# Kernel optimization log

Measured on AMD Instinct MI355X. Metric: run time of the kernel, lower is better.

The kernel has to match this reference:

```python
import jax, jax.numpy as jnp
import numpy as np

C, B, N, IN, OUT = 32, 32, 4096, 16, 32
NUM_ITERS = 3


def _squash(t, axis=-1):
    # scale = |t|^2 / (1 + |t|^2); out = scale * t / |t|
    sn = jnp.sum(t * t, axis=axis, keepdims=True)
    return (sn / (1.0 + sn)) * t / jnp.sqrt(sn)


def setup_inputs() -> dict:
    key = jax.random.key(0)
    k1, k2 = jax.random.split(key)
    x = jax.random.normal(k1, (B, N, IN), dtype=jnp.float32)
    route_weights = jax.random.normal(k2, (C, N, IN, OUT), dtype=jnp.float32)
    return {"x": x, "route_weights": route_weights}


def reference(x, route_weights):
    # priors[c,b,n,d] = sum_i x[b,n,i] * W[c,n,i,d]  (torch: [C,B,N,1,D], singleton dropped)
    priors = jnp.einsum('bni,cnio->cbno', x, route_weights)  # [C,B,N,D]
    # torch logits are [C,B,N,1,D] but constant over D (delta broadcasts), and the
    # custom softmax normalizes over dim=2 (route nodes N), so [C,B,N] is equivalent.
    logits = jnp.zeros(priors.shape[:3], dtype=priors.dtype)  # [C,B,N]
    outputs = None
    for i in range(NUM_ITERS):
        probs = jax.nn.softmax(logits, axis=2)  # softmax over route nodes (dim=2)
        s = jnp.sum(probs[..., None] * priors, axis=2, keepdims=True)  # [C,B,1,D]
        outputs = _squash(s, axis=-1)
        if i != NUM_ITERS - 1:
            logits = logits + jnp.sum(priors * outputs, axis=-1)  # agreement [C,B,N]
    return outputs[:, :, :, None, :]  # [C,B,1,1,D] to match torch output shape
```

## Files before the change

### kernel.cpp

```cpp
#include <hip/hip_runtime.h>
#include <hip/hip_cooperative_groups.h>
#include <math.h>

namespace cg = cooperative_groups;


typedef _Float16 f16x8 __attribute__((ext_vector_type(8)));
typedef float f32x16 __attribute__((ext_vector_type(16)));

namespace {
constexpr int kC = 32, kB = 32, kN = 4096, kI = 16, kD = 32;
constexpr int CHUNKS = 32;
constexpr int CHUNK_N = kN / CHUNKS;
constexpr int PS = kB * kD + kB;
constexpr int GRID = kC * CHUNKS;
constexpr size_t XT_ELEMS = (size_t)kN * kB * kI;
constexpr size_t WT_ELEMS = (size_t)kC * kN * kI * kD;
constexpr size_t P_FLOATS = (size_t)kC * CHUNKS * PS;
constexpr size_t CV_FLOATS = (size_t)kC * kB * kD;
constexpr size_t WS_BYTES_MID = XT_ELEMS * 2 + (P_FLOATS + CV_FLOATS) * 4;
constexpr size_t WS_BYTES_BIG =
    (XT_ELEMS + WT_ELEMS) * 2 + (P_FLOATS + CV_FLOATS) * 4;
constexpr size_t WS_BYTES_COOP =
    (XT_ELEMS + WT_ELEMS) * 2 + (3 * P_FLOATS + 2 * CV_FLOATS) * 4;
}

__device__ __forceinline__ f32x16 zero16() {
  f32x16 z;
#pragma unroll
  for (int r = 0; r < 16; ++r) z[r] = 0.f;
  return z;
}

__global__ __launch_bounds__(256) void k_xt(const float* __restrict__ x,
                                            _Float16* __restrict__ xt) {
  const int t = blockIdx.x * 256 + threadIdx.x;
  const int r = t >> 1, half = t & 1;
  const int b = r >> 12, n = r & 4095;
  const float4* s4 =
      reinterpret_cast<const float4*>(x) + (size_t)r * 4 + half * 2;
  const float4 f0 = s4[0], f1 = s4[1];
  f16x8 o;
  o[0] = (_Float16)f0.x; o[1] = (_Float16)f0.y;
  o[2] = (_Float16)f0.z; o[3] = (_Float16)f0.w;
  o[4] = (_Float16)f1.x; o[5] = (_Float16)f1.y;
  o[6] = (_Float16)f1.z; o[7] = (_Float16)f1.w;
  *reinterpret_cast<f16x8*>(xt + ((size_t)n * kB + b) * kI + half * 8) = o;
}


__device__ __forceinline__ void mega_sweep0(const float* __restrict__ W,
                                            const _Float16* __restrict__ xt,
                                            _Float16* __restrict__ Wt,
                                            float* __restrict__ P,
                                            float (*red)[32][33], int c,
                                            int chunk, int tid) {
  const int w = tid >> 6, l = tid & 63;
  const int m = l & 31, h = l >> 5;
  const int n0 = chunk * CHUNK_N;
  constexpr int TILES = CHUNK_N / 4;

  const float* wp = W + ((size_t)c * kN + n0 + w) * 512 + (h * 8) * 32 + m;
  const _Float16* xp = xt + ((size_t)(n0 + w)) * 512 + m * 16 + h * 8;
  _Float16* wtp = Wt + ((size_t)c * kN + n0 + w) * 512 + (size_t)l * 8;

  f32x16 accA = zero16(), accB = zero16();

  float rA0[8], rA1[8];
  f16x8 B0, B1;
#pragma unroll
  for (int j = 0; j < 8; ++j) rA0[j] = __builtin_nontemporal_load(wp + j * 32);
  B0 = *reinterpret_cast<const f16x8*>(xp);
#pragma unroll
  for (int j = 0; j < 8; ++j)
    rA1[j] = __builtin_nontemporal_load(wp + 2048 + j * 32);
  B1 = *reinterpret_cast<const f16x8*>(xp + 2048);

#pragma unroll 1
  for (int t = 0; t < TILES; t += 2) {
    {
      f16x8 a;
#pragma unroll
      for (int j = 0; j < 8; ++j) a[j] = (_Float16)rA0[j];
      const f16x8 b = B0;
      const int tn = (t + 2 < TILES) ? t + 2 : 0;
#pragma unroll
      for (int j = 0; j < 8; ++j)
        rA0[j] = __builtin_nontemporal_load(wp + (size_t)tn * 2048 + j * 32);
      B0 = *reinterpret_cast<const f16x8*>(xp + (size_t)tn * 2048);
      *reinterpret_cast<f16x8*>(wtp + (size_t)t * 2048) = a;
      accA = __builtin_amdgcn_mfma_f32_32x32x16_f16(a, b, accA, 0, 0, 0);
    }
    {
      f16x8 a;
#pragma unroll
      for (int j = 0; j < 8; ++j) a[j] = (_Float16)rA1[j];
      const f16x8 b = B1;
      const int tn = (t + 3 < TILES) ? t + 3 : 0;
#pragma unroll
      for (int j = 0; j < 8; ++j)
        rA1[j] = __builtin_nontemporal_load(wp + (size_t)tn * 2048 + j * 32);
      B1 = *reinterpret_cast<const f16x8*>(xp + (size_t)tn * 2048);
      *reinterpret_cast<f16x8*>(wtp + (size_t)(t + 1) * 2048) = a;
      accB = __builtin_amdgcn_mfma_f32_32x32x16_f16(a, b, accB, 0, 0, 0);
    }
  }
#pragma unroll
  for (int r = 0; r < 16; ++r) accA[r] += accB[r];

#pragma unroll
  for (int r = 0; r < 16; ++r)
    red[w][(r & 3) + 8 * (r >> 2) + 4 * h][m] = accA[r];
  __syncthreads();

  float* Pp = P + ((size_t)c * CHUNKS + chunk) * PS;
#pragma unroll
  for (int e = tid; e < 1024; e += 256) {
    const int d = e >> 5, bb = e & 31;
    Pp[e] = red[0][d][bb] + red[1][d][bb] + red[2][d][bb] + red[3][d][bb];
  }
  __syncthreads();
}

__device__ __forceinline__ void mega_sweep_wt(
    const _Float16* __restrict__ Wt, const _Float16* __restrict__ xt,
    const float* __restrict__ cumVec, float* __restrict__ P,
    float (*red)[32][33], float (*lred)[32], int c, int chunk, int tid) {
  const int w = tid >> 6, l = tid & 63;
  const int m = l & 31, h = l >> 5;
  const int n0 = chunk * CHUNK_N;
  constexpr int TILES = CHUNK_N / 4;

  const _Float16* wp = Wt + ((size_t)c * kN + n0 + w) * 512 + (size_t)l * 8;
  const _Float16* xp = xt + ((size_t)(n0 + w)) * 512 + m * 16 + h * 8;

  float cvr[16];
  const float* cvp = cumVec + (size_t)c * 1024 + m * 32;
#pragma unroll
  for (int r = 0; r < 16; ++r) cvr[r] = cvp[(r & 3) + 8 * (r >> 2) + 4 * h];

  f32x16 accA = zero16(), accB = zero16();
  float lacc = 0.f;
  const f32x16 z = zero16();

  f16x8 A0, A1, B0, B1;
  A0 = *reinterpret_cast<const f16x8*>(wp);
  B0 = *reinterpret_cast<const f16x8*>(xp);
  A1 = *reinterpret_cast<const f16x8*>(wp + 2048);
  B1 = *reinterpret_cast<const f16x8*>(xp + 2048);

#pragma unroll 1
  for (int t = 0; t < TILES; t += 2) {
    {
      const f16x8 a = A0;
      const f16x8 b = B0;
      const int tn = (t + 2 < TILES) ? t + 2 : 0;
      A0 = *reinterpret_cast<const f16x8*>(wp + (size_t)tn * 2048);
      B0 = *reinterpret_cast<const f16x8*>(xp + (size_t)tn * 2048);
      const f32x16 pr =
          __builtin_amdgcn_mfma_f32_32x32x16_f16(a, b, z, 0, 0, 0);
      float d0 = pr[0] * cvr[0], d1 = pr[1] * cvr[1];
      float d2 = pr[2] * cvr[2], d3 = pr[3] * cvr[3];
#pragma unroll
      for (int r = 4; r < 16; r += 4) {
        d0 = fmaf(pr[r + 0], cvr[r + 0], d0);
        d1 = fmaf(pr[r + 1], cvr[r + 1], d1);
        d2 = fmaf(pr[r + 2], cvr[r + 2], d2);
        d3 = fmaf(pr[r + 3], cvr[r + 3], d3);
      }
      float dp = (d0 + d1) + (d2 + d3);
      dp += __shfl_xor(dp, 32);
      const float e = __expf(dp);
      lacc += e;
#pragma unroll
      for (int r = 0; r < 16; ++r) accA[r] = fmaf(e, pr[r], accA[r]);
    }
    {
      const f16x8 a = A1;
      const f16x8 b = B1;
      const int tn = (t + 3 < TILES) ? t + 3 : 0;
      A1 = *reinterpret_cast<const f16x8*>(wp + (size_t)tn * 2048);
      B1 = *reinterpret_cast<const f16x8*>(xp + (size_t)tn * 2048);
      const f32x16 pr =
          __builtin_amdgcn_mfma_f32_32x32x16_f16(a, b, z, 0, 0, 0);
      float d0 = pr[0] * cvr[0], d1 = pr[1] * cvr[1];
      float d2 = pr[2] * cvr[2], d3 = pr[3] * cvr[3];
#pragma unroll
      for (int r = 4; r < 16; r += 4) {
        d0 = fmaf(pr[r + 0], cvr[r + 0], d0);
        d1 = fmaf(pr[r + 1], cvr[r + 1], d1);
        d2 = fmaf(pr[r + 2], cvr[r + 2], d2);
        d3 = fmaf(pr[r + 3], cvr[r + 3], d3);
      }
      float dp = (d0 + d1) + (d2 + d3);
      dp += __shfl_xor(dp, 32);
      const float e = __expf(dp);
      lacc += e;
#pragma unroll
      for (int r = 0; r < 16; ++r) accB[r] = fmaf(e, pr[r], accB[r]);
    }
  }
#pragma unroll
  for (int r = 0; r < 16; ++r) accA[r] += accB[r];

#pragma unroll
  for (int r = 0; r < 16; ++r)
    red[w][(r & 3) + 8 * (r >> 2) + 4 * h][m] = accA[r];
  if (h == 0) lred[w][m] = lacc;
  __syncthreads();

  float* Pp = P + ((size_t)c * CHUNKS + chunk) * PS;
#pragma unroll
  for (int e = tid; e < 1024; e += 256) {
    const int d = e >> 5, bb = e & 31;
    Pp[e] = red[0][d][bb] + red[1][d][bb] + red[2][d][bb] + red[3][d][bb];
  }
  if (tid < 32)
    Pp[1024 + tid] = lred[0][tid] + lred[1][tid] + lred[2][tid] + lred[3][tid];
  __syncthreads();
}

template <int K>
__device__ __forceinline__ void mega_reduce(const float* __restrict__ P,
                                            float* __restrict__ CVout,
                                            float* __restrict__ out,
                                            float (&cvrun)[4], int c, int t) {
  const int b = t >> 3, dg = t & 7;
  const float* Pc = P + (size_t)c * CHUNKS * PS;
  float s0 = 0.f, s1 = 0.f, s2 = 0.f, s3 = 0.f, lb = 0.f;
#pragma unroll 4
  for (int ch = 0; ch < CHUNKS; ++ch) {
    const float* base = Pc + (size_t)ch * PS;
    s0 += base[(dg + 0) * 32 + b];
    s1 += base[(dg + 8) * 32 + b];
    s2 += base[(dg + 16) * 32 + b];
    s3 += base[(dg + 24) * 32 + b];
    if (K != 0 && dg == 0) lb += base[1024 + b];
  }
  float inv;
  if constexpr (K == 0) {
    inv = 1.0f / (float)kN;
  } else {
    lb = __shfl(lb, (t & 63) & 56);
    inv = 1.0f / lb;
  }
  const float v0 = s0 * inv, v1 = s1 * inv, v2 = s2 * inv, v3 = s3 * inv;
  float sn = v0 * v0 + v1 * v1 + v2 * v2 + v3 * v3;
  sn += __shfl_xor(sn, 1);
  sn += __shfl_xor(sn, 2);
  sn += __shfl_xor(sn, 4);
  const float coef = sqrtf(sn) / (1.0f + sn);
  const size_t o0 = (size_t)c * 1024 + b * 32 + dg;
  if constexpr (K == 0) {
    cvrun[0] = v0 * coef; cvrun[1] = v1 * coef;
    cvrun[2] = v2 * coef; cvrun[3] = v3 * coef;
    CVout[o0 + 0] = cvrun[0];  CVout[o0 + 8] = cvrun[1];
    CVout[o0 + 16] = cvrun[2]; CVout[o0 + 24] = cvrun[3];
  } else if constexpr (K == 1) {
    cvrun[0] += v0 * coef; cvrun[1] += v1 * coef;
    cvrun[2] += v2 * coef; cvrun[3] += v3 * coef;
    CVout[o0 + 0] = cvrun[0];  CVout[o0 + 8] = cvrun[1];
    CVout[o0 + 16] = cvrun[2]; CVout[o0 + 24] = cvrun[3];
  } else {
    out[o0 + 0] = v0 * coef;  out[o0 + 8] = v1 * coef;
    out[o0 + 16] = v2 * coef; out[o0 + 24] = v3 * coef;
  }
}

__global__ __launch_bounds__(256, 4) void k_mega(
    const float* __restrict__ W, const _Float16* __restrict__ xt,
    _Float16* __restrict__ Wt, float* __restrict__ P0, float* __restrict__ P1,
    float* __restrict__ P2, float* __restrict__ CVa, float* __restrict__ CVb,
    float* __restrict__ out) {
  __shared__ float red[4][32][33];
  __shared__ float lred[4][32];
  cg::grid_group grid = cg::this_grid();
  const int bid = blockIdx.x;
  const int c = bid & 31;
  const int chunk = bid >> 5;
  const int tid = threadIdx.x;
  float cvrun[4] = {0.f, 0.f, 0.f, 0.f};

  mega_sweep0(W, xt, Wt, P0, red, c, chunk, tid);
  __threadfence();
  grid.sync();

  if (bid < 32) mega_reduce<0>(P0, CVa, nullptr, cvrun, bid, tid);
  __threadfence();
  grid.sync();

  mega_sweep_wt(Wt, xt, CVa, P1, red, lred, c, chunk, tid);
  __threadfence();
  grid.sync();

  if (bid < 32) mega_reduce<1>(P1, CVb, nullptr, cvrun, bid, tid);
  __threadfence();
  grid.sync();

  mega_sweep_wt(Wt, xt, CVb, P2, red, lred, c, chunk, tid);
  __threadfence();
  grid.sync();

  if (bid < 32) mega_reduce<2>(P2, nullptr, out, cvrun, bid, tid);
}


template <int MODE, bool EMIT>
__global__ __launch_bounds__(256) void k_sweep(const float* __restrict__ W,
                                               const _Float16* __restrict__ xt,
                                               const float* __restrict__ cumVec,
                                               float* __restrict__ partials,
                                               _Float16* __restrict__ Wt) {
  __shared__ float red[4][32][33];
  __shared__ float lred[4][32];
  const int bid = blockIdx.x;
  const int c = bid & 31;
  const int chunk = bid >> 5;
  const int tid = threadIdx.x;
  const int w = tid >> 6, l = tid & 63;
  const int m = l & 31, h = l >> 5;
  const int n0 = chunk * CHUNK_N;
  constexpr int TILES = CHUNK_N / 4;

  const float* wp = W + ((size_t)c * kN + n0 + w) * 512 + (h * 8) * 32 + m;
  const _Float16* xp = xt + ((size_t)(n0 + w)) * 512 + m * 16 + h * 8;
  _Float16* wtp =
      EMIT ? (Wt + ((size_t)c * kN + n0 + w) * 512 + (size_t)l * 8) : nullptr;

  float cvr[16];
  if (MODE) {
    const float* cvp = cumVec + (size_t)c * 1024 + m * 32;
#pragma unroll
    for (int r = 0; r < 16; ++r) cvr[r] = cvp[(r & 3) + 8 * (r >> 2) + 4 * h];
  }

  f32x16 accA = zero16(), accB = zero16();
  float lacc = 0.f;
  const f32x16 z = zero16();

  float rA0[8], rA1[8];
  f16x8 B0, B1;
#pragma unroll
  for (int j = 0; j < 8; ++j)
    rA0[j] = EMIT ? __builtin_nontemporal_load(wp + j * 32) : wp[j * 32];
  B0 = *reinterpret_cast<const f16x8*>(xp);
#pragma unroll
  for (int j = 0; j < 8; ++j)
    rA1[j] = EMIT ? __builtin_nontemporal_load(wp + 2048 + j * 32)
                  : wp[2048 + j * 32];
  B1 = *reinterpret_cast<const f16x8*>(xp + 2048);

#pragma unroll 1
  for (int t = 0; t < TILES; t += 2) {
    {
      f16x8 a;
#pragma unroll
      for (int j = 0; j < 8; ++j) a[j] = (_Float16)rA0[j];
      const f16x8 b = B0;
      const int tn = (t + 2 < TILES) ? t + 2 : 0;
#pragma unroll
      for (int j = 0; j < 8; ++j)
        rA0[j] = EMIT ? __builtin_nontemporal_load(wp + (size_t)tn * 2048 +
                                                   j * 32)
                      : wp[(size_t)tn * 2048 + j * 32];
      B0 = *reinterpret_cast<const f16x8*>(xp + (size_t)tn * 2048);
      if constexpr (EMIT)
        *reinterpret_cast<f16x8*>(wtp + (size_t)t * 2048) = a;
      if constexpr (MODE == 0) {
        accA = __builtin_amdgcn_mfma_f32_32x32x16_f16(a, b, accA, 0, 0, 0);
      } else {
        const f32x16 pr =
            __builtin_amdgcn_mfma_f32_32x32x16_f16(a, b, z, 0, 0, 0);
        float d0 = pr[0] * cvr[0], d1 = pr[1] * cvr[1];
        float d2 = pr[2] * cvr[2], d3 = pr[3] * cvr[3];
#pragma unroll
        for (int r = 4; r < 16; r += 4) {
          d0 = fmaf(pr[r + 0], cvr[r + 0], d0);
          d1 = fmaf(pr[r + 1], cvr[r + 1], d1);
          d2 = fmaf(pr[r + 2], cvr[r + 2], d2);
          d3 = fmaf(pr[r + 3], cvr[r + 3], d3);
        }
        float dp = (d0 + d1) + (d2 + d3);
        dp += __shfl_xor(dp, 32);
        const float e = __expf(dp);
        lacc += e;
#pragma unroll
        for (int r = 0; r < 16; ++r) accA[r] = fmaf(e, pr[r], accA[r]);
      }
    }
    {
      f16x8 a;
#pragma unroll
      for (int j = 0; j < 8; ++j) a[j] = (_Float16)rA1[j];
      const f16x8 b = B1;
      const int tn = (t + 3 < TILES) ? t + 3 : 0;
#pragma unroll
      for (int j = 0; j < 8; ++j)
        rA1[j] = EMIT ? __builtin_nontemporal_load(wp + (size_t)tn * 2048 +
                                                   j * 32)
                      : wp[(size_t)tn * 2048 + j * 32];
      B1 = *reinterpret_cast<const f16x8*>(xp + (size_t)tn * 2048);
      if constexpr (EMIT)
        *reinterpret_cast<f16x8*>(wtp + (size_t)(t + 1) * 2048) = a;
      if constexpr (MODE == 0) {
        accB = __builtin_amdgcn_mfma_f32_32x32x16_f16(a, b, accB, 0, 0, 0);
      } else {
        const f32x16 pr =
            __builtin_amdgcn_mfma_f32_32x32x16_f16(a, b, z, 0, 0, 0);
        float d0 = pr[0] * cvr[0], d1 = pr[1] * cvr[1];
        float d2 = pr[2] * cvr[2], d3 = pr[3] * cvr[3];
#pragma unroll
        for (int r = 4; r < 16; r += 4) {
          d0 = fmaf(pr[r + 0], cvr[r + 0], d0);
          d1 = fmaf(pr[r + 1], cvr[r + 1], d1);
          d2 = fmaf(pr[r + 2], cvr[r + 2], d2);
          d3 = fmaf(pr[r + 3], cvr[r + 3], d3);
        }
        float dp = (d0 + d1) + (d2 + d3);
        dp += __shfl_xor(dp, 32);
        const float e = __expf(dp);
        lacc += e;
#pragma unroll
        for (int r = 0; r < 16; ++r) accB[r] = fmaf(e, pr[r], accB[r]);
      }
    }
  }
#pragma unroll
  for (int r = 0; r < 16; ++r) accA[r] += accB[r];

#pragma unroll
  for (int r = 0; r < 16; ++r)
    red[w][(r & 3) + 8 * (r >> 2) + 4 * h][m] = accA[r];
  if (MODE && h == 0) lred[w][m] = lacc;
  __syncthreads();

  float* Pp = partials + ((size_t)c * CHUNKS + chunk) * PS;
#pragma unroll
  for (int e = tid; e < 1024; e += 256) {
    const int d = e >> 5, bb = e & 31;
    Pp[e] = red[0][d][bb] + red[1][d][bb] + red[2][d][bb] + red[3][d][bb];
  }
  if (MODE && tid < 32)
    Pp[1024 + tid] = lred[0][tid] + lred[1][tid] + lred[2][tid] + lred[3][tid];
}

__global__ __launch_bounds__(256) void k_sweep_wt(
    const _Float16* __restrict__ Wt, const _Float16* __restrict__ xt,
    const float* __restrict__ cumVec, float* __restrict__ partials) {
  __shared__ float red[4][32][33];
  __shared__ float lred[4][32];
  const int bid = blockIdx.x;
  const int c = bid & 31;
  const int chunk = bid >> 5;
  const int tid = threadIdx.x;
  mega_sweep_wt(Wt, xt, cumVec, partials, red, lred, c, chunk, tid);
}

template <int K>
__global__ __launch_bounds__(1024) void k_reduce(
    const float* __restrict__ partials, float* __restrict__ CV,
    float* __restrict__ out) {
  const int c = blockIdx.x;
  const int t = threadIdx.x;
  const int b = t >> 5, d = t & 31;
  const float* Pc = partials + (size_t)c * CHUNKS * PS;
  float s = 0.f;
#pragma unroll 4
  for (int ch = 0; ch < CHUNKS; ++ch) s += Pc[(size_t)ch * PS + d * 32 + b];
  float inv;
  if constexpr (K == 0) {
    inv = 1.0f / (float)kN;
  } else {
    float lb = 0.f;
#pragma unroll 4
    for (int ch = 0; ch < CHUNKS; ++ch) lb += Pc[(size_t)ch * PS + 1024 + b];
    inv = 1.0f / lb;
  }
  const float sv = s * inv;
  float sn = sv * sv;
  sn += __shfl_xor(sn, 1);
  sn += __shfl_xor(sn, 2);
  sn += __shfl_xor(sn, 4);
  sn += __shfl_xor(sn, 8);
  sn += __shfl_xor(sn, 16);
  const float coef = sqrtf(sn) / (1.0f + sn);
  const float o = sv * coef;
  if constexpr (K == 2)
    out[(size_t)c * 1024 + t] = o;
  else if constexpr (K == 0)
    CV[(size_t)c * 1024 + t] = o;
  else
    CV[(size_t)c * 1024 + t] += o;
}

namespace v1 {
constexpr int BG = 4, NSLOT = 128, THREADS1 = NSLOT * 8;
template <int MODE>
__device__ __forceinline__ void sweep_pass(const float* __restrict__ Wc,
                                           const float* __restrict__ x, int b0,
                                           int tid, int nslot, int dg,
                                           float (*red)[8][20], float (*sS)[kD],
                                           float* sL, const float (*sVec)[kD]) {
  float acc[BG][4];
  float lv[BG];
#pragma unroll
  for (int b = 0; b < BG; ++b) {
    lv[b] = 0.f;
#pragma unroll
    for (int j = 0; j < 4; ++j) acc[b][j] = 0.f;
  }
  float vec[BG][4];
  if (MODE) {
#pragma unroll
    for (int b = 0; b < BG; ++b)
#pragma unroll
      for (int j = 0; j < 4; ++j) vec[b][j] = sVec[b][4 * dg + j];
  }
#pragma unroll 1
  for (int n = nslot; n < kN; n += NSLOT) {
    const float* Wn = Wc + (size_t)n * (kI * kD) + 4 * dg;
    float pr[BG][4];
#pragma unroll
    for (int b = 0; b < BG; ++b)
#pragma unroll
      for (int j = 0; j < 4; ++j) pr[b][j] = 0.f;
#pragma unroll
    for (int iq = 0; iq < 4; ++iq) {
      float4 wv[4];
#pragma unroll
      for (int r = 0; r < 4; ++r)
        wv[r] = *reinterpret_cast<const float4*>(Wn + (4 * iq + r) * kD);
#pragma unroll
      for (int b = 0; b < BG; ++b) {
        const float4 xv = *reinterpret_cast<const float4*>(
            x + ((size_t)(b0 + b) * kN + n) * kI + 4 * iq);
        const float xsv[4] = {xv.x, xv.y, xv.z, xv.w};
#pragma unroll
        for (int r = 0; r < 4; ++r) {
          pr[b][0] = fmaf(xsv[r], wv[r].x, pr[b][0]);
          pr[b][1] = fmaf(xsv[r], wv[r].y, pr[b][1]);
          pr[b][2] = fmaf(xsv[r], wv[r].z, pr[b][2]);
          pr[b][3] = fmaf(xsv[r], wv[r].w, pr[b][3]);
        }
      }
    }
    if (MODE == 0) {
#pragma unroll
      for (int b = 0; b < BG; ++b)
#pragma unroll
        for (int j = 0; j < 4; ++j) acc[b][j] += pr[b][j];
    } else {
#pragma unroll
      for (int b = 0; b < BG; ++b) {
        float dp = pr[b][0] * vec[b][0] + pr[b][1] * vec[b][1] +
                   pr[b][2] * vec[b][2] + pr[b][3] * vec[b][3];
        dp += __shfl_xor(dp, 1);
        dp += __shfl_xor(dp, 2);
        dp += __shfl_xor(dp, 4);
        const float e = __expf(dp);
        lv[b] += e;
        acc[b][0] = fmaf(e, pr[b][0], acc[b][0]);
        acc[b][1] = fmaf(e, pr[b][1], acc[b][1]);
        acc[b][2] = fmaf(e, pr[b][2], acc[b][2]);
        acc[b][3] = fmaf(e, pr[b][3], acc[b][3]);
      }
    }
  }
#pragma unroll
  for (int b = 0; b < BG; ++b) {
#pragma unroll
    for (int j = 0; j < 4; ++j) {
      float v = acc[b][j];
      v += __shfl_xor(v, 8);
      v += __shfl_xor(v, 16);
      v += __shfl_xor(v, 32);
      acc[b][j] = v;
    }
    if (MODE) {
      float v = lv[b];
      v += __shfl_xor(v, 8);
      v += __shfl_xor(v, 16);
      v += __shfl_xor(v, 32);
      lv[b] = v;
    }
  }
  const int lane = tid & 63;
  const int wv_id = tid >> 6;
  if ((lane >> 3) == 0) {
#pragma unroll
    for (int b = 0; b < BG; ++b) {
#pragma unroll
      for (int j = 0; j < 4; ++j) red[wv_id][dg][4 * b + j] = acc[b][j];
      if (MODE) red[wv_id][dg][16 + b] = lv[b];
    }
  }
  __syncthreads();
  if (tid < 128) {
    const int dgc = tid >> 4, e = tid & 15;
    float s = 0.f;
#pragma unroll
    for (int w = 0; w < 16; ++w) s += red[w][dgc][e];
    sS[e >> 2][4 * dgc + (e & 3)] = s;
  }
  if (MODE && tid >= 128 && tid < 128 + BG) {
    const int b = tid - 128;
    float s = 0.f;
#pragma unroll
    for (int w = 0; w < 16; ++w) s += red[w][0][16 + b];
    sL[b] = s;
  }
  __syncthreads();
}

__global__ __launch_bounds__(THREADS1, 4) void caps_route_kernel(
    const float* __restrict__ x, const float* __restrict__ W,
    float* __restrict__ out) {
  __shared__ float red[16][8][20];
  __shared__ float sS[BG][kD];
  __shared__ float sVec[BG][kD];
  __shared__ float sL[BG];
  const int i = blockIdx.x;
  const int xcd = i & 7;
  const int j = i >> 3;
  const int c = xcd + 8 * (j >> 3);
  const int b0 = 4 * (j & 7);
  const int tid = threadIdx.x;
  const int nslot = tid >> 3;
  const int dg = tid & 7;
  const float* Wc = W + (size_t)c * kN * kI * kD;
  sweep_pass<0>(Wc, x, b0, tid, nslot, dg, red, sS, sL, sVec);
  if (tid < BG) {
    const int b = tid;
    float sval[kD], sn = 0.f;
    const float inv = 1.0f / (float)kN;
#pragma unroll
    for (int d = 0; d < kD; ++d) {
      sval[d] = sS[b][d] * inv;
      sn += sval[d] * sval[d];
    }
    const float coef = sqrtf(sn) / (1.0f + sn);
#pragma unroll
    for (int d = 0; d < kD; ++d) sVec[b][d] = sval[d] * coef;
  }
  __syncthreads();
  sweep_pass<1>(Wc, x, b0, tid, nslot, dg, red, sS, sL, sVec);
  if (tid < BG) {
    const int b = tid;
    float sval[kD], sn = 0.f;
    const float inv = 1.0f / sL[b];
#pragma unroll
    for (int d = 0; d < kD; ++d) {
      sval[d] = sS[b][d] * inv;
      sn += sval[d] * sval[d];
    }
    const float coef = sqrtf(sn) / (1.0f + sn);
#pragma unroll
    for (int d = 0; d < kD; ++d) sVec[b][d] += sval[d] * coef;
  }
  __syncthreads();
  sweep_pass<1>(Wc, x, b0, tid, nslot, dg, red, sS, sL, sVec);
  if (tid < BG) {
    const int b = tid;
    float sval[kD], sn = 0.f;
    const float inv = 1.0f / sL[b];
#pragma unroll
    for (int d = 0; d < kD; ++d) {
      sval[d] = sS[b][d] * inv;
      sn += sval[d] * sval[d];
    }
    const float coef = sqrtf(sn) / (1.0f + sn);
    float* o = out + ((size_t)c * kB + (b0 + b)) * kD;
#pragma unroll
    for (int d = 0; d < kD; ++d) o[d] = sval[d] * coef;
  }
}
}

extern "C" void kernel_launch(void* const* d_in, const int* in_sizes, int n_in,
                              void* d_out, int out_size, void* d_ws,
                              size_t ws_size, hipStream_t stream) {
  const float* x = (const float*)d_in[0];
  const float* W = (const float*)d_in[1];
  float* out = (float*)d_out;
  (void)in_sizes; (void)n_in; (void)out_size;

  static int s_coop = -1;
  if (s_coop < 0) {
    int dev = 0;
    (void)hipGetDevice(&dev);
    int nCU = 0;
    (void)hipDeviceGetAttribute(&nCU, hipDeviceAttributeMultiprocessorCount,
                                dev);
    int maxB = 0;
    (void)hipOccupancyMaxActiveBlocksPerMultiprocessor(&maxB, k_mega, 256, 0);
    s_coop = (nCU > 0 && maxB > 0 && (size_t)nCU * maxB >= (size_t)GRID) ? 1
                                                                         : 0;
  }

  if (s_coop == 1 && ws_size >= WS_BYTES_COOP) {
    _Float16* xt = (_Float16*)d_ws;
    _Float16* Wt = xt + XT_ELEMS;
    float* P0 = (float*)(Wt + WT_ELEMS);
    float* P1 = P0 + P_FLOATS;
    float* P2 = P1 + P_FLOATS;
    float* CVa = P2 + P_FLOATS;
    float* CVb = CVa + CV_FLOATS;

    k_xt<<<GRID, 256, 0, stream>>>(x, xt);
    void* args[] = {(void*)&W,  (void*)&xt,  (void*)&Wt,
                    (void*)&P0, (void*)&P1,  (void*)&P2,
                    (void*)&CVa, (void*)&CVb, (void*)&out};
    if (hipLaunchCooperativeKernel(k_mega, dim3(GRID), dim3(256), args, 0,
                                   stream) == hipSuccess)
      return;
  }

  if (ws_size >= WS_BYTES_BIG) {
    _Float16* xt = (_Float16*)d_ws;
    _Float16* Wt = xt + XT_ELEMS;
    float* P = (float*)(Wt + WT_ELEMS);
    float* CV = P + P_FLOATS;

    k_xt<<<GRID, 256, 0, stream>>>(x, xt);
    k_sweep<0, true><<<GRID, 256, 0, stream>>>(W, xt, nullptr, P, Wt);
    k_reduce<0><<<kC, 1024, 0, stream>>>(P, CV, nullptr);
    k_sweep_wt<<<GRID, 256, 0, stream>>>(Wt, xt, CV, P);
    k_reduce<1><<<kC, 1024, 0, stream>>>(P, CV, nullptr);
    k_sweep_wt<<<GRID, 256, 0, stream>>>(Wt, xt, CV, P);
    k_reduce<2><<<kC, 1024, 0, stream>>>(P, nullptr, out);
    return;
  }

  if (ws_size >= WS_BYTES_MID) {
    _Float16* xt = (_Float16*)d_ws;
    float* P = (float*)(xt + XT_ELEMS);
    float* CV = P + P_FLOATS;

    k_xt<<<GRID, 256, 0, stream>>>(x, xt);
    k_sweep<0, false><<<GRID, 256, 0, stream>>>(W, xt, nullptr, P, nullptr);
    k_reduce<0><<<kC, 1024, 0, stream>>>(P, CV, nullptr);
    k_sweep<1, false><<<GRID, 256, 0, stream>>>(W, xt, CV, P, nullptr);
    k_reduce<1><<<kC, 1024, 0, stream>>>(P, CV, nullptr);
    k_sweep<1, false><<<GRID, 256, 0, stream>>>(W, xt, CV, P, nullptr);
    k_reduce<2><<<kC, 1024, 0, stream>>>(P, nullptr, out);
    return;
  }

  v1::caps_route_kernel<<<256, v1::THREADS1, 0, stream>>>(x, W, out);
}
```

Measured before the change: 200.9 us.

## Replace cooperative grid syncs with per-capsule atomic barriers and redundant reductions

The cooperative-launch grid.sync barriers are replaced by a hand-built two-level atomic counter barrier, reset by the xt conversion kernel. Every block now redundantly reduces its own capsule's partials into shared memory, so the separate reduce phase and its extra grid barrier go away. Only the final output reduction waits again, and only in chunk-0 blocks. This removes barrier overhead and the serialized reduce stage, at the cost of redundant reduction reads and reliance on all blocks being co-resident under a normal launch.

```diff
diff --git a/kernel.cpp b/kernel.cpp
--- a/kernel.cpp
+++ b/kernel.cpp
@@ -1,8 +1,5 @@
 #include <hip/hip_runtime.h>
-#include <hip/hip_cooperative_groups.h>
 #include <math.h>
-
-namespace cg = cooperative_groups;
 
 
 typedef _Float16 f16x8 __attribute__((ext_vector_type(8)));
@@ -18,11 +15,12 @@
 constexpr size_t WT_ELEMS = (size_t)kC * kN * kI * kD;
 constexpr size_t P_FLOATS = (size_t)kC * CHUNKS * PS;
 constexpr size_t CV_FLOATS = (size_t)kC * kB * kD;
+constexpr int BAR_U32 = 33;
 constexpr size_t WS_BYTES_MID = XT_ELEMS * 2 + (P_FLOATS + CV_FLOATS) * 4;
 constexpr size_t WS_BYTES_BIG =
     (XT_ELEMS + WT_ELEMS) * 2 + (P_FLOATS + CV_FLOATS) * 4;
-constexpr size_t WS_BYTES_COOP =
-    (XT_ELEMS + WT_ELEMS) * 2 + (3 * P_FLOATS + 2 * CV_FLOATS) * 4;
+constexpr size_t WS_BYTES_MEGA =
+    (XT_ELEMS + WT_ELEMS) * 2 + 3 * P_FLOATS * 4 + 256;
 }
 
 __device__ __forceinline__ f32x16 zero16() {
@@ -33,7 +31,9 @@
 }
 
 __global__ __launch_bounds__(256) void k_xt(const float* __restrict__ x,
-                                            _Float16* __restrict__ xt) {
+                                            _Float16* __restrict__ xt,
+                                            unsigned* __restrict__ bar) {
+  if (bar && blockIdx.x == 0 && threadIdx.x < BAR_U32) bar[threadIdx.x] = 0u;
   const int t = blockIdx.x * 256 + threadIdx.x;
   const int r = t >> 1, half = t & 1;
   const int b = r >> 12, n = r & 4095;
@@ -48,6 +48,29 @@
   *reinterpret_cast<f16x8*>(xt + ((size_t)n * kB + b) * kI + half * 8) = o;
 }
 
+__device__ __forceinline__ void bar_arrive(unsigned* bar, int bid, int tid) {
+  __threadfence();
+  __syncthreads();
+  if (tid == 0) {
+    const int g = bid & 31;
+    unsigned v = __hip_atomic_fetch_add(&bar[g], 1u, __ATOMIC_ACQ_REL,
+                                        __HIP_MEMORY_SCOPE_AGENT);
+    if ((v & 31u) == 31u)
+      __hip_atomic_fetch_add(&bar[32], 1u, __ATOMIC_ACQ_REL,
+                             __HIP_MEMORY_SCOPE_AGENT);
+  }
+}
+
+__device__ __forceinline__ void bar_wait(unsigned* bar, int tid, int epoch) {
+  if (tid == 0) {
+    const unsigned target = 32u * (unsigned)epoch;
+    while (__hip_atomic_load(&bar[32], __ATOMIC_ACQUIRE,
+                             __HIP_MEMORY_SCOPE_AGENT) < target)
+      __builtin_amdgcn_s_sleep(2);
+  }
+  __syncthreads();
+}
+
 
 __device__ __forceinline__ void mega_sweep0(const float* __restrict__ W,
                                             const _Float16* __restrict__ xt,
@@ -119,13 +142,12 @@
     const int d = e >> 5, bb = e & 31;
     Pp[e] = red[0][d][bb] + red[1][d][bb] + red[2][d][bb] + red[3][d][bb];
   }
-  __syncthreads();
 }
 
 __device__ __forceinline__ void mega_sweep_wt(
     const _Float16* __restrict__ Wt, const _Float16* __restrict__ xt,
-    const float* __restrict__ cumVec, float* __restrict__ P,
-    float (*red)[32][33], float (*lred)[32], int c, int chunk, int tid) {
+    const float (*sCV)[32], float* __restrict__ P, float (*red)[32][33],
+    float (*lred)[32], int c, int chunk, int tid) {
   const int w = tid >> 6, l = tid & 63;
   const int m = l & 31, h = l >> 5;
   const int n0 = chunk * CHUNK_N;
@@ -135,9 +157,9 @@
   const _Float16* xp = xt + ((size_t)(n0 + w)) * 512 + m * 16 + h * 8;
 
   float cvr[16];
-  const float* cvp = cumVec + (size_t)c * 1024 + m * 32;
-#pragma unroll
-  for (int r = 0; r < 16; ++r) cvr[r] = cvp[(r & 3) + 8 * (r >> 2) + 4 * h];
+#pragma unroll
+  for (int r = 0; r < 16; ++r)
+    cvr[r] = sCV[m][(r & 3) + 8 * (r >> 2) + 4 * h];
 
   f32x16 accA = zero16(), accB = zero16();
   float lacc = 0.f;
@@ -217,25 +239,30 @@
   }
   if (tid < 32)
     Pp[1024 + tid] = lred[0][tid] + lred[1][tid] + lred[2][tid] + lred[3][tid];
-  __syncthreads();
 }
 
 template <int K>
 __device__ __forceinline__ void mega_reduce(const float* __restrict__ P,
-                                            float* __restrict__ CVout,
                                             float* __restrict__ out,
-                                            float (&cvrun)[4], int c, int t) {
+                                            float (&cvrun)[4],
+                                            float (*sCV)[32], int c, int t) {
   const int b = t >> 3, dg = t & 7;
   const float* Pc = P + (size_t)c * CHUNKS * PS;
   float s0 = 0.f, s1 = 0.f, s2 = 0.f, s3 = 0.f, lb = 0.f;
 #pragma unroll 4
   for (int ch = 0; ch < CHUNKS; ++ch) {
     const float* base = Pc + (size_t)ch * PS;
-    s0 += base[(dg + 0) * 32 + b];
-    s1 += base[(dg + 8) * 32 + b];
-    s2 += base[(dg + 16) * 32 + b];
-    s3 += base[(dg + 24) * 32 + b];
-    if (K != 0 && dg == 0) lb += base[1024 + b];
+    s0 += __hip_atomic_load(base + (dg + 0) * 32 + b, __ATOMIC_RELAXED,
+                            __HIP_MEMORY_SCOPE_AGENT);
+    s1 += __hip_atomic_load(base + (dg + 8) * 32 + b, __ATOMIC_RELAXED,
+                            __HIP_MEMORY_SCOPE_AGENT);
+    s2 += __hip_atomic_load(base + (dg + 16) * 32 + b, __ATOMIC_RELAXED,
+                            __HIP_MEMORY_SCOPE_AGENT);
+    s3 += __hip_atomic_load(base + (dg + 24) * 32 + b, __ATOMIC_RELAXED,
+                            __HIP_MEMORY_SCOPE_AGENT);
+    if (K != 0 && dg == 0)
+      lb += __hip_atomic_load(base + 1024 + b, __ATOMIC_RELAXED,
+                              __HIP_MEMORY_SCOPE_AGENT);
   }
   float inv;
   if constexpr (K == 0) {
@@ -250,31 +277,31 @@
   sn += __shfl_xor(sn, 2);
   sn += __shfl_xor(sn, 4);
   const float coef = sqrtf(sn) / (1.0f + sn);
-  const size_t o0 = (size_t)c * 1024 + b * 32 + dg;
-  if constexpr (K == 0) {
-    cvrun[0] = v0 * coef; cvrun[1] = v1 * coef;
-    cvrun[2] = v2 * coef; cvrun[3] = v3 * coef;
-    CVout[o0 + 0] = cvrun[0];  CVout[o0 + 8] = cvrun[1];
-    CVout[o0 + 16] = cvrun[2]; CVout[o0 + 24] = cvrun[3];
-  } else if constexpr (K == 1) {
-    cvrun[0] += v0 * coef; cvrun[1] += v1 * coef;
-    cvrun[2] += v2 * coef; cvrun[3] += v3 * coef;
-    CVout[o0 + 0] = cvrun[0];  CVout[o0 + 8] = cvrun[1];
-    CVout[o0 + 16] = cvrun[2]; CVout[o0 + 24] = cvrun[3];
-  } else {
+  if constexpr (K == 2) {
+    const size_t o0 = (size_t)c * 1024 + b * 32 + dg;
     out[o0 + 0] = v0 * coef;  out[o0 + 8] = v1 * coef;
     out[o0 + 16] = v2 * coef; out[o0 + 24] = v3 * coef;
-  }
-}
-
-__global__ __launch_bounds__(256, 4) void k_mega(
+  } else {
+    if constexpr (K == 0) {
+      cvrun[0] = v0 * coef; cvrun[1] = v1 * coef;
+      cvrun[2] = v2 * coef; cvrun[3] = v3 * coef;
+    } else {
+      cvrun[0] += v0 * coef; cvrun[1] += v1 * coef;
+      cvrun[2] += v2 * coef; cvrun[3] += v3 * coef;
+    }
+    sCV[b][dg + 0] = cvrun[0];  sCV[b][dg + 8] = cvrun[1];
+    sCV[b][dg + 16] = cvrun[2]; sCV[b][dg + 24] = cvrun[3];
+  }
+}
+
+__global__ __launch_bounds__(256, 4) void k_mega2(
     const float* __restrict__ W, const _Float16* __restrict__ xt,
     _Float16* __restrict__ Wt, float* __restrict__ P0, float* __restrict__ P1,
-    float* __restrict__ P2, float* __restrict__ CVa, float* __restrict__ CVb,
+    float* __restrict__ P2, unsigned* __restrict__ bar,
     float* __restrict__ out) {
   __shared__ float red[4][32][33];
   __shared__ float lred[4][32];
-  cg::grid_group grid = cg::this_grid();
+  __shared__ float sCV[32][32];
   const int bid = blockIdx.x;
   const int c = bid & 31;
   const int chunk = bid >> 5;
@@ -282,26 +309,26 @@
   float cvrun[4] = {0.f, 0.f, 0.f, 0.f};
 
   mega_sweep0(W, xt, Wt, P0, red, c, chunk, tid);
-  __threadfence();
-  grid.sync();
-
-  if (bid < 32) mega_reduce<0>(P0, CVa, nullptr, cvrun, bid, tid);
-  __threadfence();
-  grid.sync();
-
-  mega_sweep_wt(Wt, xt, CVa, P1, red, lred, c, chunk, tid);
-  __threadfence();
-  grid.sync();
-
-  if (bid < 32) mega_reduce<1>(P1, CVb, nullptr, cvrun, bid, tid);
-  __threadfence();
-  grid.sync();
-
-  mega_sweep_wt(Wt, xt, CVb, P2, red, lred, c, chunk, tid);
-  __threadfence();
-  grid.sync();
-
-  if (bid < 32) mega_reduce<2>(P2, nullptr, out, cvrun, bid, tid);
+  bar_arrive(bar, bid, tid);
+  bar_wait(bar, tid, 1);
+
+  mega_reduce<0>(P0, nullptr, cvrun, sCV, c, tid);
+  __syncthreads();
+
+  mega_sweep_wt(Wt, xt, sCV, P1, red, lred, c, chunk, tid);
+  bar_arrive(bar, bid, tid);
+  bar_wait(bar, tid, 2);
+
+  mega_reduce<1>(P1, nullptr, cvrun, sCV, c, tid);
+  __syncthreads();
+
+  mega_sweep_wt(Wt, xt, sCV, P2, red, lred, c, chunk, tid);
+  bar_arrive(bar, bid, tid);
+
+  if (chunk == 0) {
+    bar_wait(bar, tid, 3);
+    mega_reduce<2>(P2, out, cvrun, sCV, c, tid);
+  }
 }
 
 
@@ -449,11 +476,15 @@
     const float* __restrict__ cumVec, float* __restrict__ partials) {
   __shared__ float red[4][32][33];
   __shared__ float lred[4][32];
+  __shared__ float sCV[32][32];
   const int bid = blockIdx.x;
   const int c = bid & 31;
   const int chunk = bid >> 5;
   const int tid = threadIdx.x;
-  mega_sweep_wt(Wt, xt, cumVec, partials, red, lred, c, chunk, tid);
+  for (int e = tid; e < 1024; e += 256)
+    sCV[e >> 5][e & 31] = cumVec[(size_t)c * 1024 + e];
+  __syncthreads();
+  mega_sweep_wt(Wt, xt, sCV, partials, red, lred, c, chunk, tid);
 }
 
 template <int K>
@@ -684,35 +715,31 @@
   float* out = (float*)d_out;
   (void)in_sizes; (void)n_in; (void)out_size;
 
-  static int s_coop = -1;
-  if (s_coop < 0) {
+  static int s_mega = -1;
+  if (s_mega < 0) {
     int dev = 0;
     (void)hipGetDevice(&dev);
     int nCU = 0;
     (void)hipDeviceGetAttribute(&nCU, hipDeviceAttributeMultiprocessorCount,
                                 dev);
     int maxB = 0;
-    (void)hipOccupancyMaxActiveBlocksPerMultiprocessor(&maxB, k_mega, 256, 0);
-    s_coop = (nCU > 0 && maxB > 0 && (size_t)nCU * maxB >= (size_t)GRID) ? 1
-                                                                         : 0;
-  }
-
-  if (s_coop == 1 && ws_size >= WS_BYTES_COOP) {
+    (void)hipOccupancyMaxActiveBlocksPerMultiprocessor(&maxB, k_mega2, 256, 0);
+    s_mega = (nCU > 0 && maxB > 0 && (size_t)nCU * (size_t)maxB >= (size_t)GRID)
+                 ? 1
+                 : 0;
+  }
+
+  if (s_mega == 1 && ws_size >= WS_BYTES_MEGA) {
     _Float16* xt = (_Float16*)d_ws;
     _Float16* Wt = xt + XT_ELEMS;
     float* P0 = (float*)(Wt + WT_ELEMS);
     float* P1 = P0 + P_FLOATS;
     float* P2 = P1 + P_FLOATS;
-    float* CVa = P2 + P_FLOATS;
-    float* CVb = CVa + CV_FLOATS;
-
-    k_xt<<<GRID, 256, 0, stream>>>(x, xt);
-    void* args[] = {(void*)&W,  (void*)&xt,  (void*)&Wt,
-                    (void*)&P0, (void*)&P1,  (void*)&P2,
-                    (void*)&CVa, (void*)&CVb, (void*)&out};
-    if (hipLaunchCooperativeKernel(k_mega, dim3(GRID), dim3(256), args, 0,
-                                   stream) == hipSuccess)
-      return;
+    unsigned* bar = (unsigned*)(P2 + P_FLOATS);
+
+    k_xt<<<GRID, 256, 0, stream>>>(x, xt, bar);
+    k_mega2<<<GRID, 256, 0, stream>>>(W, xt, Wt, P0, P1, P2, bar, out);
+    return;
   }
 
   if (ws_size >= WS_BYTES_BIG) {
@@ -721,7 +748,7 @@
     float* P = (float*)(Wt + WT_ELEMS);
     float* CV = P + P_FLOATS;
 
-    k_xt<<<GRID, 256, 0, stream>>>(x, xt);
+    k_xt<<<GRID, 256, 0, stream>>>(x, xt, nullptr);
     k_sweep<0, true><<<GRID, 256, 0, stream>>>(W, xt, nullptr, P, Wt);
     k_reduce<0><<<kC, 1024, 0, stream>>>(P, CV, nullptr);
     k_sweep_wt<<<GRID, 256, 0, stream>>>(Wt, xt, CV, P);
@@ -736,7 +763,7 @@
     float* P = (float*)(xt + XT_ELEMS);
     float* CV = P + P_FLOATS;
 
-    k_xt<<<GRID, 256, 0, stream>>>(x, xt);
+    k_xt<<<GRID, 256, 0, stream>>>(x, xt, nullptr);
     k_sweep<0, false><<<GRID, 256, 0, stream>>>(W, xt, nullptr, P, nullptr);
     k_reduce<0><<<kC, 1024, 0, stream>>>(P, CV, nullptr);
     k_sweep<1, false><<<GRID, 256, 0, stream>>>(W, xt, CV, P, nullptr);
```

After: 200.7 us. About the same (-0.1%).
